# Kernel optimization log

Hardware: AMD Instinct MI355X
Metric: run time of the kernel (lower is better)

Reference implementation:

```python
import jax, jax.numpy as jnp
import numpy as np

N_NODES = 100000
DIM = 128
N_EDGES = 1600000
BN_EPS = 1e-5


def setup_inputs() -> dict:
    key = jax.random.key(0)
    ks = jax.random.split(key, 8)
    x = jax.random.normal(ks[0], (N_NODES, DIM), dtype=jnp.float32)
    ei = jax.random.randint(ks[1], (2, N_EDGES), 0, N_NODES, dtype=jnp.int32)
    # GINConv train_eps scalar
    eps = jnp.zeros((), dtype=jnp.float32)
    # MLP: Linear(dim, 2*dim) -> BN(2*dim) -> ReLU -> Dropout -> Linear(2*dim, dim) -> BN(dim) -> ReLU
    s1 = 1.0 / np.sqrt(DIM)
    s2 = 1.0 / np.sqrt(2 * DIM)
    W1 = jax.random.uniform(ks[2], (DIM, 2 * DIM), jnp.float32, -s1, s1)
    b1 = jax.random.uniform(ks[3], (2 * DIM,), jnp.float32, -s1, s1)
    W2 = jax.random.uniform(ks[4], (2 * DIM, DIM), jnp.float32, -s2, s2)
    b2 = jax.random.uniform(ks[5], (DIM,), jnp.float32, -s2, s2)
    g1 = jnp.ones((2 * DIM,), jnp.float32)
    be1 = jnp.zeros((2 * DIM,), jnp.float32)
    m1 = jax.random.normal(ks[6], (2 * DIM,), jnp.float32) * 0.1
    v1 = jnp.ones((2 * DIM,), jnp.float32)
    g2 = jnp.ones((DIM,), jnp.float32)
    be2 = jnp.zeros((DIM,), jnp.float32)
    m2 = jax.random.normal(ks[7], (DIM,), jnp.float32) * 0.1
    v2 = jnp.ones((DIM,), jnp.float32)
    return {"x": x, "eps": eps, "W1": W1, "b1": b1, "g1": g1, "be1": be1,
            "m1": m1, "v1": v1, "W2": W2, "b2": b2, "g2": g2, "be2": be2,
            "m2": m2, "v2": v2, "ei": ei}


def _bn(h, gamma, beta, mean, var):
    # BatchNorm1d in eval mode (running stats)
    return gamma * (h - mean) * jax.lax.rsqrt(var + BN_EPS) + beta


def reference(x, eps, W1, b1, g1, be1, m1, v1, W2, b2, g2, be2, m2, v2, ei):
    src, dst = ei[0], ei[1]
    # GIN aggregation: sum of neighbor (source) features scattered to destination
    agg = jax.ops.segment_sum(x[src], dst, num_segments=N_NODES)  # [N, dim]
    h = (1.0 + eps) * x + agg
    h = jax.nn.relu(_bn(h @ W1 + b1, g1, be1, m1, v1))  # [N, 2*dim]
    # Dropout is identity in eval mode
    h = jax.nn.relu(_bn(h @ W2 + b2, g2, be2, m2, v2))  # [N, dim]
    return h
```

## Files before the change

kernel.cpp:

```cpp
#include <hip/hip_runtime.h>

#define N_NODES 100000
#define DIM     128
#define HID     256
#define BN_EPS  1e-5f
#define TILES   3125
#define GEMM_GRID 256
#define BK_BITS 9
#define NBK     196
#define BKCAP   12288
#define EPB     4096
#define CVT_BLOCKS 3125

typedef _Float16     half8  __attribute__((ext_vector_type(8)));
typedef float        f32x4  __attribute__((ext_vector_type(4)));

static __device__ __forceinline__ f32x4 mfma16h(half8 a, half8 b, f32x4 c) {
    return __builtin_amdgcn_mfma_f32_16x16x32_f16(a, b, c, 0, 0, 0);
}

__global__ __launch_bounds__(256) void binscatter_kernel(
    const int* __restrict__ src, const int* __restrict__ dst,
    int* __restrict__ cursor, unsigned int* __restrict__ pairs, int nE) {
    __shared__ int cnt[NBK];
    __shared__ int gbase[NBK];
    int t = threadIdx.x;
    for (int i = t; i < NBK; i += 256) cnt[i] = 0;
    __syncthreads();
    int e0 = blockIdx.x * EPB;
    int n = min(EPB, nE - e0);
    int d[16];
#pragma unroll
    for (int k = 0; k < 16; ++k) {
        int idx = t + k * 256;
        if (idx < n) {
            d[k] = dst[e0 + idx];
            atomicAdd(&cnt[d[k] >> BK_BITS], 1);
        }
    }
    __syncthreads();
    for (int i = t; i < NBK; i += 256) {
        int c = cnt[i];
        gbase[i] = c ? atomicAdd(&cursor[i], c) : 0;
    }
    __syncthreads();
    for (int i = t; i < NBK; i += 256) cnt[i] = 0;
    __syncthreads();
#pragma unroll
    for (int k = 0; k < 16; ++k) {
        int idx = t + k * 256;
        if (idx < n) {
            int b = d[k] >> BK_BITS;
            int r = atomicAdd(&cnt[b], 1);
            pairs[(long long)b * BKCAP + gbase[b] + r] =
                ((unsigned)src[e0 + idx] << BK_BITS) | ((unsigned)d[k] & 511u);
        }
    }
}

__global__ __launch_bounds__(512) void fill_cvt_kernel(
    const unsigned int* __restrict__ pairs, const int* __restrict__ cursor,
    int* __restrict__ rowptr, int* __restrict__ csr_src,
    const float* __restrict__ x, _Float16* __restrict__ x16) {
    int t = threadIdx.x;
    if (blockIdx.x >= NBK) {
        int bc = blockIdx.x - NBK;
#pragma unroll
        for (int k = 0; k < 2; ++k) {
            int i = bc * 1024 + k * 512 + t;
            float4 v = ((const float4*)x)[i];
            _Float16 h0 = (_Float16)v.x, h1 = (_Float16)v.y,
                     h2 = (_Float16)v.z, h3 = (_Float16)v.w;
            unsigned long long pk =
                (unsigned long long)__builtin_bit_cast(unsigned short, h0)
              | ((unsigned long long)__builtin_bit_cast(unsigned short, h1) << 16)
              | ((unsigned long long)__builtin_bit_cast(unsigned short, h2) << 32)
              | ((unsigned long long)__builtin_bit_cast(unsigned short, h3) << 48);
            ((unsigned long long*)x16)[i] = pk;
        }
        return;
    }
    __shared__ int cnt[512];
    __shared__ int off[512];
    __shared__ int stmp[256];
    __shared__ int s_base;
    int b = blockIdx.x;
    if (t < 256) stmp[t] = (t < NBK) ? cursor[t] : 0;
    __syncthreads();
    for (int s = 1; s < 256; s <<= 1) {
        int a = (t >= s && t < 256) ? stmp[t - s] : 0;
        __syncthreads();
        if (t < 256) stmp[t] += a;
        __syncthreads();
    }
    if (t == 0) s_base = stmp[b] - cursor[b];
    __syncthreads();
    int base = s_base;
    int m = cursor[b];
    int nd0 = b << BK_BITS;
    int nn = min(512, N_NODES - nd0);
    const unsigned int* bp = pairs + (long long)b * BKCAP;
    cnt[t] = 0;
    __syncthreads();
    for (int e = t; e < m; e += 512)
        atomicAdd(&cnt[bp[e] & 511u], 1);
    __syncthreads();
    int v = cnt[t];
    off[t] = v;
    __syncthreads();
    for (int s = 1; s < 512; s <<= 1) {
        int a = (t >= s) ? off[t - s] : 0;
        __syncthreads();
        off[t] += a;
        __syncthreads();
    }
    int excl = off[t] - v;
    __syncthreads();
    off[t] = excl;
    if (t < nn) rowptr[nd0 + t] = base + excl;
    if (b == NBK - 1 && t == 0) rowptr[N_NODES] = base + m;
    cnt[t] = 0;
    __syncthreads();
    for (int e = t; e < m; e += 512) {
        unsigned int p = bp[e];
        int li = p & 511u;
        int r = atomicAdd(&cnt[li], 1);
        csr_src[base + off[li] + r] = (int)(p >> BK_BITS);
    }
}

__global__ __launch_bounds__(256) void gather_kernel(
    const _Float16* __restrict__ x16, const float* __restrict__ epsp,
    const int* __restrict__ rowptr, const int* __restrict__ csr_src,
    _Float16* __restrict__ h16) {
    int node = blockIdx.x * 16 + (threadIdx.x >> 4);
    int lane = threadIdx.x & 15;
    const half8* xp = (const half8*)x16;
    int beg = rowptr[node], end = rowptr[node + 1];
    float s[8] = {0,0,0,0,0,0,0,0};
    int j = beg;
    for (; j + 8 <= end; j += 8) {
        int n0 = csr_src[j],   n1 = csr_src[j+1], n2 = csr_src[j+2], n3 = csr_src[j+3];
        int n4 = csr_src[j+4], n5 = csr_src[j+5], n6 = csr_src[j+6], n7 = csr_src[j+7];
        half8 v0 = xp[n0 * 16 + lane];
        half8 v1 = xp[n1 * 16 + lane];
        half8 v2 = xp[n2 * 16 + lane];
        half8 v3 = xp[n3 * 16 + lane];
        half8 v4 = xp[n4 * 16 + lane];
        half8 v5 = xp[n5 * 16 + lane];
        half8 v6 = xp[n6 * 16 + lane];
        half8 v7 = xp[n7 * 16 + lane];
#pragma unroll
        for (int i = 0; i < 8; ++i) {
            float a = ((float)v0[i] + (float)v1[i]) + ((float)v2[i] + (float)v3[i]);
            float b = ((float)v4[i] + (float)v5[i]) + ((float)v6[i] + (float)v7[i]);
            s[i] += a + b;
        }
    }
    for (; j < end; ++j) {
        half8 v = xp[csr_src[j] * 16 + lane];
#pragma unroll
        for (int i = 0; i < 8; ++i) s[i] += (float)v[i];
    }
    float sc = 1.f + epsp[0];
    half8 xv = xp[node * 16 + lane];
    half8 o;
#pragma unroll
    for (int i = 0; i < 8; ++i) o[i] = (_Float16)fmaf(sc, (float)xv[i], s[i]);
    ((half8*)h16)[node * 16 + lane] = o;
}

__global__ __launch_bounds__(512, 2) void mlp_fused_kernel(
    const _Float16* __restrict__ h16,
    const float* __restrict__ W1, const float* __restrict__ b1,
    const float* __restrict__ g1, const float* __restrict__ be1,
    const float* __restrict__ m1, const float* __restrict__ v1,
    const float* __restrict__ W2, const float* __restrict__ b2,
    const float* __restrict__ g2, const float* __restrict__ be2,
    const float* __restrict__ m2, const float* __restrict__ v2,
    float* __restrict__ out) {
    __shared__ _Float16 sh1[32 * HID];
    int t = threadIdx.x;
    int w = t >> 6, l = t & 63;
    int l15 = l & 15, q = l >> 4;
    int cg = w & 3, mg = w >> 2;

    half8 B1[4][4];
    float s1v[4], sh1v[4];
#pragma unroll
    for (int nt = 0; nt < 4; ++nt) {
        int col = 64 * cg + 16 * nt + l15;
#pragma unroll
        for (int ks = 0; ks < 4; ++ks) {
            half8 bh;
#pragma unroll
            for (int i = 0; i < 8; ++i)
                bh[i] = (_Float16)W1[(32 * ks + 8 * q + i) * HID + col];
            B1[nt][ks] = bh;
        }
        float sc = g1[col] * rsqrtf(v1[col] + BN_EPS);
        s1v[nt] = sc;
        sh1v[nt] = (b1[col] - m1[col]) * sc + be1[col];
    }
    half8 B2[2][8];
    float s2v[2], sh2v[2];
#pragma unroll
    for (int nt = 0; nt < 2; ++nt) {
        int col = 32 * cg + 16 * nt + l15;
#pragma unroll
        for (int ks = 0; ks < 8; ++ks) {
            half8 bh;
#pragma unroll
            for (int i = 0; i < 8; ++i)
                bh[i] = (_Float16)W2[(32 * ks + 8 * q + i) * DIM + col];
            B2[nt][ks] = bh;
        }
        float sc = g2[col] * rsqrtf(v2[col] + BN_EPS);
        s2v[nt] = sc;
        sh2v[nt] = (b2[col] - m2[col]) * sc + be2[col];
    }

    for (int tile = blockIdx.x; tile < TILES; tile += GEMM_GRID) {
        int row0 = tile * 32;
        const _Float16* arow = h16 + (long long)(row0 + 16 * mg + l15) * DIM;
        half8 A[4];
#pragma unroll
        for (int ks = 0; ks < 4; ++ks) A[ks] = *(const half8*)(arow + 32 * ks + 8 * q);
        f32x4 acc[4];
#pragma unroll
        for (int nt = 0; nt < 4; ++nt) acc[nt] = (f32x4)(0.f);
#pragma unroll
        for (int nt = 0; nt < 4; ++nt)
#pragma unroll
            for (int ks = 0; ks < 4; ++ks)
                acc[nt] = mfma16h(A[ks], B1[nt][ks], acc[nt]);
#pragma unroll
        for (int nt = 0; nt < 4; ++nt) {
            int col = 64 * cg + 16 * nt + l15;
#pragma unroll
            for (int reg = 0; reg < 4; ++reg) {
                int row = 16 * mg + 4 * q + reg;
                float vv = fmaxf(0.f, fmaf(acc[nt][reg], s1v[nt], sh1v[nt]));
                sh1[row * HID + (col ^ ((row & 7) << 3))] = (_Float16)vv;
            }
        }
        __syncthreads();
        half8 A2[8];
        {
            int row = 16 * mg + l15;
            int sx = (row & 7) << 3;
#pragma unroll
            for (int ks = 0; ks < 8; ++ks)
                A2[ks] = *(const half8*)&sh1[row * HID + ((32 * ks + 8 * q) ^ sx)];
        }
        __syncthreads();
        f32x4 acc2[2];
        acc2[0] = (f32x4)(0.f); acc2[1] = (f32x4)(0.f);
#pragma unroll
        for (int nt = 0; nt < 2; ++nt)
#pragma unroll
            for (int ks = 0; ks < 8; ++ks)
                acc2[nt] = mfma16h(A2[ks], B2[nt][ks], acc2[nt]);
#pragma unroll
        for (int nt = 0; nt < 2; ++nt) {
            int col = 32 * cg + 16 * nt + l15;
#pragma unroll
            for (int reg = 0; reg < 4; ++reg) {
                int orow = row0 + 16 * mg + 4 * q + reg;
                out[(long long)orow * DIM + col] =
                    fmaxf(0.f, fmaf(acc2[nt][reg], s2v[nt], sh2v[nt]));
            }
        }
    }
}

extern "C" void kernel_launch(void* const* d_in, const int* in_sizes, int n_in,
                              void* d_out, int out_size, void* d_ws, size_t ws_size,
                              hipStream_t stream) {
    const float* x   = (const float*)d_in[0];
    const float* eps = (const float*)d_in[1];
    const float* W1  = (const float*)d_in[2];
    const float* b1  = (const float*)d_in[3];
    const float* g1  = (const float*)d_in[4];
    const float* be1 = (const float*)d_in[5];
    const float* m1  = (const float*)d_in[6];
    const float* v1  = (const float*)d_in[7];
    const float* W2  = (const float*)d_in[8];
    const float* b2  = (const float*)d_in[9];
    const float* g2  = (const float*)d_in[10];
    const float* be2 = (const float*)d_in[11];
    const float* m2  = (const float*)d_in[12];
    const float* v2  = (const float*)d_in[13];
    const int*   ei  = (const int*)d_in[14];
    int nE = in_sizes[14] / 2;
    const int* src = ei;
    const int* dst = ei + nE;

    char* ws = (char*)d_ws;
    int*          cursor  = (int*)(ws + 0);
    int*          rowptr  = (int*)(ws + 4096);
    int*          csr_src = (int*)(ws + 405504);
    unsigned int* pairs   = (unsigned int*)(ws + 6806528);
    _Float16*     x16     = (_Float16*)(ws + 16441344);
    _Float16*     h16     = (_Float16*)(ws + 42041344);

    hipMemsetAsync(cursor, 0, NBK * sizeof(int), stream);
    binscatter_kernel<<<(nE + EPB - 1) / EPB, 256, 0, stream>>>(src, dst, cursor, pairs, nE);

    fill_cvt_kernel<<<NBK + CVT_BLOCKS, 512, 0, stream>>>(pairs, cursor, rowptr, csr_src,
                                                          x, x16);

    gather_kernel<<<N_NODES / 16, 256, 0, stream>>>(x16, eps, rowptr, csr_src, h16);

    mlp_fused_kernel<<<GEMM_GRID, 512, 0, stream>>>(h16, W1, b1, g1, be1, m1, v1,
                                                    W2, b2, g2, be2, m2, v2, (float*)d_out);
}
```

Baseline: 154.4 us.

## Spread each node's gather over a full wavefront and shrink MLP tiles

The gather kernel now gives each node a 64-lane wavefront: four 16-lane groups each handle different neighbors, and the partial sums are combined with cross-lane shuffles. This is meant to cut per-node serial latency and balance uneven degrees better than one 16-lane group walking the whole neighbor list. The MLP kernel changes from 512-thread blocks on 32-row tiles to 256-thread blocks on 16-row tiles, with a larger grid and half the shared memory. The cost is the shuffle reduction, three quarters of the lanes idle during the final write, and each block reloading the weights into registers.

```diff
diff --git a/kernel.cpp b/kernel.cpp
--- a/kernel.cpp
+++ b/kernel.cpp
@@ -4,8 +4,8 @@
 #define DIM     128
 #define HID     256
 #define BN_EPS  1e-5f
-#define TILES   3125
-#define GEMM_GRID 256
+#define TILES16 6250
+#define MLP_GRID 512
 #define BK_BITS 9
 #define NBK     196
 #define BKCAP   12288
@@ -133,44 +133,49 @@
     const _Float16* __restrict__ x16, const float* __restrict__ epsp,
     const int* __restrict__ rowptr, const int* __restrict__ csr_src,
     _Float16* __restrict__ h16) {
-    int node = blockIdx.x * 16 + (threadIdx.x >> 4);
-    int lane = threadIdx.x & 15;
+    int node = blockIdx.x * 4 + (threadIdx.x >> 6);
+    int lane = threadIdx.x & 63;
+    int g = lane >> 4;
+    int part = lane & 15;
     const half8* xp = (const half8*)x16;
     int beg = rowptr[node], end = rowptr[node + 1];
     float s[8] = {0,0,0,0,0,0,0,0};
     int j = beg;
     for (; j + 8 <= end; j += 8) {
-        int n0 = csr_src[j],   n1 = csr_src[j+1], n2 = csr_src[j+2], n3 = csr_src[j+3];
-        int n4 = csr_src[j+4], n5 = csr_src[j+5], n6 = csr_src[j+6], n7 = csr_src[j+7];
-        half8 v0 = xp[n0 * 16 + lane];
-        half8 v1 = xp[n1 * 16 + lane];
-        half8 v2 = xp[n2 * 16 + lane];
-        half8 v3 = xp[n3 * 16 + lane];
-        half8 v4 = xp[n4 * 16 + lane];
-        half8 v5 = xp[n5 * 16 + lane];
-        half8 v6 = xp[n6 * 16 + lane];
-        half8 v7 = xp[n7 * 16 + lane];
-#pragma unroll
-        for (int i = 0; i < 8; ++i) {
-            float a = ((float)v0[i] + (float)v1[i]) + ((float)v2[i] + (float)v3[i]);
-            float b = ((float)v4[i] + (float)v5[i]) + ((float)v6[i] + (float)v7[i]);
-            s[i] += a + b;
-        }
-    }
-    for (; j < end; ++j) {
-        half8 v = xp[csr_src[j] * 16 + lane];
+        int n0 = csr_src[j + g];
+        int n1 = csr_src[j + 4 + g];
+        half8 v0 = xp[n0 * 16 + part];
+        half8 v1 = xp[n1 * 16 + part];
+#pragma unroll
+        for (int i = 0; i < 8; ++i) s[i] += (float)v0[i] + (float)v1[i];
+    }
+    int r = end - j;
+    if (g < r) {
+        half8 v = xp[csr_src[j + g] * 16 + part];
 #pragma unroll
         for (int i = 0; i < 8; ++i) s[i] += (float)v[i];
     }
-    float sc = 1.f + epsp[0];
-    half8 xv = xp[node * 16 + lane];
-    half8 o;
-#pragma unroll
-    for (int i = 0; i < 8; ++i) o[i] = (_Float16)fmaf(sc, (float)xv[i], s[i]);
-    ((half8*)h16)[node * 16 + lane] = o;
-}
-
-__global__ __launch_bounds__(512, 2) void mlp_fused_kernel(
+    if (g + 4 < r) {
+        half8 v = xp[csr_src[j + 4 + g] * 16 + part];
+#pragma unroll
+        for (int i = 0; i < 8; ++i) s[i] += (float)v[i];
+    }
+#pragma unroll
+    for (int i = 0; i < 8; ++i) {
+        s[i] += __shfl_xor(s[i], 16);
+        s[i] += __shfl_xor(s[i], 32);
+    }
+    if (lane < 16) {
+        float sc = 1.f + epsp[0];
+        half8 xv = xp[node * 16 + part];
+        half8 o;
+#pragma unroll
+        for (int i = 0; i < 8; ++i) o[i] = (_Float16)fmaf(sc, (float)xv[i], s[i]);
+        ((half8*)h16)[node * 16 + part] = o;
+    }
+}
+
+__global__ __launch_bounds__(256, 2) void mlp_fused_kernel(
     const _Float16* __restrict__ h16,
     const float* __restrict__ W1, const float* __restrict__ b1,
     const float* __restrict__ g1, const float* __restrict__ be1,
@@ -179,11 +184,10 @@
     const float* __restrict__ g2, const float* __restrict__ be2,
     const float* __restrict__ m2, const float* __restrict__ v2,
     float* __restrict__ out) {
-    __shared__ _Float16 sh1[32 * HID];
+    __shared__ _Float16 sh1[16 * HID];
     int t = threadIdx.x;
-    int w = t >> 6, l = t & 63;
+    int cg = t >> 6, l = t & 63;
     int l15 = l & 15, q = l >> 4;
-    int cg = w & 3, mg = w >> 2;
 
     half8 B1[4][4];
     float s1v[4], sh1v[4];
@@ -220,9 +224,9 @@
         sh2v[nt] = (b2[col] - m2[col]) * sc + be2[col];
     }
 
-    for (int tile = blockIdx.x; tile < TILES; tile += GEMM_GRID) {
-        int row0 = tile * 32;
-        const _Float16* arow = h16 + (long long)(row0 + 16 * mg + l15) * DIM;
+    for (int tile = blockIdx.x; tile < TILES16; tile += MLP_GRID) {
+        int row0 = tile * 16;
+        const _Float16* arow = h16 + (long long)(row0 + l15) * DIM;
         half8 A[4];
 #pragma unroll
         for (int ks = 0; ks < 4; ++ks) A[ks] = *(const half8*)(arow + 32 * ks + 8 * q);
@@ -239,7 +243,7 @@
             int col = 64 * cg + 16 * nt + l15;
 #pragma unroll
             for (int reg = 0; reg < 4; ++reg) {
-                int row = 16 * mg + 4 * q + reg;
+                int row = 4 * q + reg;
                 float vv = fmaxf(0.f, fmaf(acc[nt][reg], s1v[nt], sh1v[nt]));
                 sh1[row * HID + (col ^ ((row & 7) << 3))] = (_Float16)vv;
             }
@@ -247,7 +251,7 @@
         __syncthreads();
         half8 A2[8];
         {
-            int row = 16 * mg + l15;
+            int row = l15;
             int sx = (row & 7) << 3;
 #pragma unroll
             for (int ks = 0; ks < 8; ++ks)
@@ -266,7 +270,7 @@
             int col = 32 * cg + 16 * nt + l15;
 #pragma unroll
             for (int reg = 0; reg < 4; ++reg) {
-                int orow = row0 + 16 * mg + 4 * q + reg;
+                int orow = row0 + 4 * q + reg;
                 out[(long long)orow * DIM + col] =
                     fmaxf(0.f, fmaf(acc2[nt][reg], s2v[nt], sh2v[nt]));
             }
@@ -310,8 +314,8 @@
     fill_cvt_kernel<<<NBK + CVT_BLOCKS, 512, 0, stream>>>(pairs, cursor, rowptr, csr_src,
                                                           x, x16);
 
-    gather_kernel<<<N_NODES / 16, 256, 0, stream>>>(x16, eps, rowptr, csr_src, h16);
-
-    mlp_fused_kernel<<<GEMM_GRID, 512, 0, stream>>>(h16, W1, b1, g1, be1, m1, v1,
-                                                    W2, b2, g2, be2, m2, v2, (float*)d_out);
-}
+    gather_kernel<<<N_NODES / 4, 256, 0, stream>>>(x16, eps, rowptr, csr_src, h16);
+
+    mlp_fused_kernel<<<MLP_GRID, 256, 0, stream>>>(h16, W1, b1, g1, be1, m1, v1,
+                                                   W2, b2, g2, be2, m2, v2, (float*)d_out);
+}
```

Result: faster. 149.6 us (-3.1%).
